# Performance work log

Hardware: AMD Instinct MI355X
Metric: run time of the kernel (lower is better)

## Reference

```python
import jax, jax.numpy as jnp
import numpy as np

N = 100000          # nodes
E = 3200000         # edges (before self-loops)
F_IN = 3            # num_features
H = 32              # hidden_size
F_EDGE = 4          # NUM_EDGE_FEATURES
T = 1               # target_size
SLOPE = 0.2         # GATConv negative_slope default


def setup_inputs() -> dict:
    key = jax.random.key(0)
    ks = jax.random.split(key, 18)
    s = 0.1  # small init scale
    inp = {
        "x": jax.random.normal(ks[0], (N, F_IN), jnp.float32),
        "edge_index": jax.random.randint(ks[1], (2, E), 0, N, dtype=jnp.int32),
        "edge_attr": jax.random.normal(ks[2], (E, F_EDGE), jnp.float32),
        # GATConv layer 1 (in=3, out=32, heads=1, edge_dim=4)
        "W1": jax.random.normal(ks[3], (F_IN, H), jnp.float32) * s,
        "We1": jax.random.normal(ks[4], (F_EDGE, H), jnp.float32) * s,
        "a_src1": jax.random.normal(ks[5], (H,), jnp.float32) * s,
        "a_dst1": jax.random.normal(ks[6], (H,), jnp.float32) * s,
        "a_edge1": jax.random.normal(ks[7], (H,), jnp.float32) * s,
        "b1": jnp.zeros((H,), jnp.float32),
        # GATConv layer 2 (in=32, out=32)
        "W2": jax.random.normal(ks[8], (H, H), jnp.float32) * s,
        "We2": jax.random.normal(ks[9], (F_EDGE, H), jnp.float32) * s,
        "a_src2": jax.random.normal(ks[10], (H,), jnp.float32) * s,
        "a_dst2": jax.random.normal(ks[11], (H,), jnp.float32) * s,
        "a_edge2": jax.random.normal(ks[12], (H,), jnp.float32) * s,
        "b2": jnp.zeros((H,), jnp.float32),
        # final Linear(32 -> 1)
        "Wl": jax.random.normal(ks[13], (H, T), jnp.float32) * s,
        "bl": jnp.zeros((T,), jnp.float32),
    }
    return inp


def _add_self_loops(edge_index, edge_attr, n):
    # PyG GATConv default: add_self_loops=True, fill_value='mean' -> self-loop
    # edge_attr is the mean of incoming edge_attr per destination node.
    src, dst = edge_index[0], edge_index[1]
    cnt = jax.ops.segment_sum(jnp.ones((edge_attr.shape[0],), edge_attr.dtype), dst, num_segments=n)
    sums = jax.ops.segment_sum(edge_attr, dst, num_segments=n)
    loop_attr = sums / jnp.maximum(cnt, 1.0)[:, None]
    idx = jnp.arange(n, dtype=src.dtype)
    src2 = jnp.concatenate([src, idx])
    dst2 = jnp.concatenate([dst, idx])
    ea2 = jnp.concatenate([edge_attr, loop_attr], axis=0)
    return src2, dst2, ea2


def _gat_layer(x, src, dst, ea, W, We, a_src, a_dst, a_edge, bias, n):
    h = x @ W                       # [N, H]
    e = ea @ We                     # [E', H]
    logits = jax.nn.leaky_relu(h[src] @ a_src + h[dst] @ a_dst + e @ a_edge, SLOPE)  # [E']
    # softmax over edges grouped by destination node
    m = jax.ops.segment_max(logits, dst, num_segments=n)
    w = jnp.exp(logits - m[dst])
    denom = jax.ops.segment_sum(w, dst, num_segments=n)
    alpha = w / denom[dst]
    out = jax.ops.segment_sum(alpha[:, None] * h[src], dst, num_segments=n)  # [N, H]
    return out + bias


def reference(x, edge_index, edge_attr, W1, We1, a_src1, a_dst1, a_edge1, b1,
              W2, We2, a_src2, a_dst2, a_edge2, b2, Wl, bl):
    n = x.shape[0]
    src, dst, ea = _add_self_loops(edge_index, edge_attr, n)
    h = _gat_layer(x, src, dst, ea, W1, We1, a_src1, a_dst1, a_edge1, b1, n)
    h = jax.nn.relu(h)  # dropout is identity in eval mode
    h = _gat_layer(h, src, dst, ea, W2, We2, a_src2, a_dst2, a_edge2, b2, n)
    out = h @ Wl + bl
    return jax.nn.relu(out)
```

## Files before the change

### kernel.cpp

```cpp
#include <hip/hip_runtime.h>
#include <hip/hip_fp16.h>


#define NN 100000
#define EE 3200000
#define SLOPE 0.2f
#define SB 1024
#define SNB ((NN + SB - 1) / SB)

__global__ void k_small(const float* __restrict__ We1, const float* __restrict__ ae1,
                        const float* __restrict__ We2, const float* __restrict__ ae2,
                        const float* __restrict__ W1, const float* __restrict__ as1,
                        const float* __restrict__ ad1, float* __restrict__ sml) {
    int t = threadIdx.x;
    if (t < 4) {
        float s = 0.f;
        for (int k = 0; k < 32; k++) s += We1[t * 32 + k] * ae1[k];
        sml[t] = s;
    } else if (t < 8) {
        float s = 0.f;
        for (int k = 0; k < 32; k++) s += We2[(t - 4) * 32 + k] * ae2[k];
        sml[t] = s;
    } else if (t < 11) {
        int i = t - 8;
        float s = 0.f;
        for (int k = 0; k < 32; k++) s += W1[i * 32 + k] * as1[k];
        sml[t] = s;
    } else if (t < 14) {
        int i = t - 11;
        float s = 0.f;
        for (int k = 0; k < 32; k++) s += W1[i * 32 + k] * ad1[k];
        sml[t] = s;
    }
}

__global__ void k_deg(const int* __restrict__ ei, int* __restrict__ deg) {
    int e = blockIdx.x * blockDim.x + threadIdx.x;
    if (e >= EE) return;
    atomicAdd(&deg[ei[EE + e]], 1);
}

__global__ void k_scan1(const int* __restrict__ deg, int* __restrict__ loc,
                        int* __restrict__ bsum) {
    __shared__ int sd[SB];
    int t = threadIdx.x;
    int i = blockIdx.x * SB + t;
    int v = (i < NN) ? deg[i] : 0;
    sd[t] = v;
    __syncthreads();
    for (int o = 1; o < SB; o <<= 1) {
        int u = (t >= o) ? sd[t - o] : 0;
        __syncthreads();
        sd[t] += u;
        __syncthreads();
    }
    if (i < NN) loc[i] = sd[t] - v;
    if (t == SB - 1) bsum[blockIdx.x] = sd[t];
}

__global__ void k_scan2(int* __restrict__ bsum) {
    __shared__ int sd[128];
    int t = threadIdx.x;
    int v = (t < SNB) ? bsum[t] : 0;
    sd[t] = v;
    __syncthreads();
    for (int o = 1; o < 128; o <<= 1) {
        int u = (t >= o) ? sd[t - o] : 0;
        __syncthreads();
        sd[t] += u;
        __syncthreads();
    }
    if (t < SNB) bsum[t] = sd[t] - v;
}

__global__ void k_scan3(const int* __restrict__ loc, const int* __restrict__ bsum,
                        int* __restrict__ rp, int* __restrict__ cur,
                        const float* __restrict__ x, const float* __restrict__ sml,
                        float* __restrict__ hs, float* __restrict__ hd) {
    int i = blockIdx.x * blockDim.x + threadIdx.x;
    if (i > NN) return;
    if (i == NN) { rp[NN] = EE; return; }
    int p = loc[i] + bsum[i / SB];
    rp[i] = p;
    cur[i] = p;
    float x0 = x[i * 3], x1 = x[i * 3 + 1], x2 = x[i * 3 + 2];
    hs[i] = x0 * sml[8] + x1 * sml[9] + x2 * sml[10];
    hd[i] = x0 * sml[11] + x1 * sml[12] + x2 * sml[13];
}

__global__ void k_scatter(const int* __restrict__ ei, const float* __restrict__ ea,
                          const float* __restrict__ sml, int* __restrict__ cur,
                          int2* __restrict__ cpack) {
    int e = blockIdx.x * blockDim.x + threadIdx.x;
    if (e >= EE) return;
    int s = ei[e], d = ei[EE + e];
    float4 a = reinterpret_cast<const float4*>(ea)[e];
    float e1 = a.x * sml[0] + a.y * sml[1] + a.z * sml[2] + a.w * sml[3];
    float e2 = a.x * sml[4] + a.y * sml[5] + a.z * sml[6] + a.w * sml[7];
    __half2 hv = __floats2half2_rn(e1, e2);
    int2 rec;
    rec.x = s;
    rec.y = *reinterpret_cast<int*>(&hv);
    int p = atomicAdd(&cur[d], 1);
    cpack[p] = rec;
}

__global__ void k_h2(const float* __restrict__ x2, const float* __restrict__ W,
                     const float* __restrict__ as_, const float* __restrict__ ad_,
                     float* __restrict__ h, float* __restrict__ hs, float* __restrict__ hd) {
    __shared__ float sW[1024], sa[32], sdv[32];
    int t = threadIdx.x;
    for (int i = t; i < 1024; i += blockDim.x) sW[i] = W[i];
    if (t < 32) { sa[t] = as_[t]; sdv[t] = ad_[t]; }
    __syncthreads();
    int n = blockIdx.x * blockDim.x + t;
    if (n >= NN) return;
    float xl[32];
    const float4* xp = reinterpret_cast<const float4*>(x2 + (size_t)n * 32);
#pragma unroll
    for (int q = 0; q < 8; q++) {
        float4 v = xp[q];
        xl[q * 4 + 0] = v.x; xl[q * 4 + 1] = v.y; xl[q * 4 + 2] = v.z; xl[q * 4 + 3] = v.w;
    }
    float ss = 0.f, dd = 0.f;
    float* hp = h + (size_t)n * 32;
    for (int q = 0; q < 8; q++) {
        float4 o;
        float* op = (float*)&o;
        for (int j = 0; j < 4; j++) {
            int k = q * 4 + j;
            float acc = 0.f;
#pragma unroll
            for (int i = 0; i < 32; i++) acc += xl[i] * sW[i * 32 + k];
            op[j] = acc;
            ss += acc * sa[k];
            dd += acc * sdv[k];
        }
        reinterpret_cast<float4*>(hp)[q] = o;
    }
    hs[n] = ss; hd[n] = dd;
}

template <int LAYER>
__global__ void __launch_bounds__(256) k_gather(
    const int* __restrict__ rp, const int2* __restrict__ cpack,
    const float* __restrict__ hsrc,
    const float* __restrict__ W1, const float* __restrict__ hs,
    const float* __restrict__ hd, const float* __restrict__ bias,
    const float* __restrict__ Wl, const float* __restrict__ bl,
    float* __restrict__ out) {
    __shared__ float sW[96];
    if (LAYER == 0) {
        if (threadIdx.x < 96) sW[threadIdx.x] = W1[threadIdx.x];
        __syncthreads();
    }
    int wid = (blockIdx.x * blockDim.x + threadIdx.x) >> 6;
    int lane = threadIdx.x & 63;
    if (wid >= NN) return;
    int n = wid;
    int beg = rp[n], end = rp[n + 1];
    int deg = end - beg;
    float hdn = hd[n];

    float mymax = -1e30f, mysum = 0.f;
    for (int j = beg + lane; j < end; j += 64) {
        int2 cp = cpack[j];
        __half2 hv = *reinterpret_cast<__half2*>(&cp.y);
        float2 ew = __half22float2(hv);
        float eaw = (LAYER == 0) ? ew.x : ew.y;
        float l = hs[cp.x] + hdn + eaw;
        l = (l >= 0.f) ? l : SLOPE * l;
        mymax = fmaxf(mymax, l);
        mysum += eaw;
    }
#pragma unroll
    for (int o = 32; o; o >>= 1) {
        mymax = fmaxf(mymax, __shfl_xor(mymax, o));
        mysum += __shfl_xor(mysum, o);
    }
    float lself = hs[n] + hdn + mysum / fmaxf((float)deg, 1.f);
    lself = (lself >= 0.f) ? lself : SLOPE * lself;
    float m = fmaxf(mymax, lself);

    int g = lane >> 3, q = lane & 7;
    float ax = 0.f, ay = 0.f, az = 0.f, aw = 0.f, wsum = 0.f;
    for (int j = beg + g; j < end; j += 8) {
        int2 cp = cpack[j];
        __half2 hv2 = *reinterpret_cast<__half2*>(&cp.y);
        float2 ew = __half22float2(hv2);
        float eaw = (LAYER == 0) ? ew.x : ew.y;
        int s = cp.x;
        float l = hs[s] + hdn + eaw;
        l = (l >= 0.f) ? l : SLOPE * l;
        float w = __expf(l - m);
        wsum += w;
        float hx, hy, hz, hw;
        if (LAYER == 0) {
            float x0 = hsrc[s * 3], x1 = hsrc[s * 3 + 1], x2 = hsrc[s * 3 + 2];
            int k = q * 4;
            hx = x0 * sW[k + 0] + x1 * sW[32 + k + 0] + x2 * sW[64 + k + 0];
            hy = x0 * sW[k + 1] + x1 * sW[32 + k + 1] + x2 * sW[64 + k + 1];
            hz = x0 * sW[k + 2] + x1 * sW[32 + k + 2] + x2 * sW[64 + k + 2];
            hw = x0 * sW[k + 3] + x1 * sW[32 + k + 3] + x2 * sW[64 + k + 3];
        } else {
            float4 hv4 = reinterpret_cast<const float4*>(hsrc + (size_t)s * 32)[q];
            hx = hv4.x; hy = hv4.y; hz = hv4.z; hw = hv4.w;
        }
        ax += w * hx; ay += w * hy; az += w * hz; aw += w * hw;
    }
    if (g == (deg & 7)) {
        float w = __expf(lself - m);
        wsum += w;
        float hx, hy, hz, hw;
        if (LAYER == 0) {
            float x0 = hsrc[n * 3], x1 = hsrc[n * 3 + 1], x2 = hsrc[n * 3 + 2];
            int k = q * 4;
            hx = x0 * sW[k + 0] + x1 * sW[32 + k + 0] + x2 * sW[64 + k + 0];
            hy = x0 * sW[k + 1] + x1 * sW[32 + k + 1] + x2 * sW[64 + k + 1];
            hz = x0 * sW[k + 2] + x1 * sW[32 + k + 2] + x2 * sW[64 + k + 2];
            hw = x0 * sW[k + 3] + x1 * sW[32 + k + 3] + x2 * sW[64 + k + 3];
        } else {
            float4 hv4 = reinterpret_cast<const float4*>(hsrc + (size_t)n * 32)[q];
            hx = hv4.x; hy = hv4.y; hz = hv4.z; hw = hv4.w;
        }
        ax += w * hx; ay += w * hy; az += w * hz; aw += w * hw;
    }
#pragma unroll
    for (int o = 8; o < 64; o <<= 1) {
        ax += __shfl_xor(ax, o); ay += __shfl_xor(ay, o);
        az += __shfl_xor(az, o); aw += __shfl_xor(aw, o);
        wsum += __shfl_xor(wsum, o);
    }
    float inv = 1.f / wsum;
    if (LAYER == 0) {
        if (lane < 8) {
            float4 bb = reinterpret_cast<const float4*>(bias)[q];
            float4 o4;
            o4.x = fmaxf(ax * inv + bb.x, 0.f);
            o4.y = fmaxf(ay * inv + bb.y, 0.f);
            o4.z = fmaxf(az * inv + bb.z, 0.f);
            o4.w = fmaxf(aw * inv + bb.w, 0.f);
            reinterpret_cast<float4*>(out + (size_t)n * 32)[q] = o4;
        }
    } else {
        float4 bb = reinterpret_cast<const float4*>(bias)[q];
        float4 wl = reinterpret_cast<const float4*>(Wl)[q];
        float part = (ax * inv + bb.x) * wl.x + (ay * inv + bb.y) * wl.y +
                     (az * inv + bb.z) * wl.z + (aw * inv + bb.w) * wl.w;
        part += __shfl_xor(part, 1);
        part += __shfl_xor(part, 2);
        part += __shfl_xor(part, 4);
        if (lane == 0) out[n] = fmaxf(part + bl[0], 0.f);
    }
}

extern "C" void kernel_launch(void* const* d_in, const int* in_sizes, int n_in,
                              void* d_out, int out_size, void* d_ws, size_t ws_size,
                              hipStream_t stream) {
    const float* x   = (const float*)d_in[0];
    const int*   ei  = (const int*)d_in[1];
    const float* ea  = (const float*)d_in[2];
    const float* W1  = (const float*)d_in[3];
    const float* We1 = (const float*)d_in[4];
    const float* as1 = (const float*)d_in[5];
    const float* ad1 = (const float*)d_in[6];
    const float* ae1 = (const float*)d_in[7];
    const float* b1  = (const float*)d_in[8];
    const float* W2  = (const float*)d_in[9];
    const float* We2 = (const float*)d_in[10];
    const float* as2 = (const float*)d_in[11];
    const float* ad2 = (const float*)d_in[12];
    const float* ae2 = (const float*)d_in[13];
    const float* b2  = (const float*)d_in[14];
    const float* Wl  = (const float*)d_in[15];
    const float* bl  = (const float*)d_in[16];
    float* out = (float*)d_out;

    const size_t n = NN, E = EE;
    float* ws = (float*)d_ws;
    int*   rp    = (int*)ws;
    int*   deg   = (int*)ws + n + 4;
    int*   cur   = (int*)ws + 2 * n + 4;
    int*   loc   = (int*)ws + 3 * n + 4;
    int*   bsum  = (int*)ws + 4 * n + 4;
    float* hs    = ws + 4 * n + 132;
    float* hd    = ws + 5 * n + 132;
    float* sml   = ws + 6 * n + 132;
    int2*  cpack = (int2*)(ws + 6 * n + 148);
    float* h     = ws + 6 * n + 148 + 2 * E;
    float* xbuf  = ws + 38 * n + 148 + 2 * E;

    dim3 b256(256);
    int gE  = (EE + 255) / 256;
    int gN  = (NN + 255) / 256;
    int gN1 = (NN + 256) / 256;
    int gG  = (NN * 64 + 255) / 256;

    hipMemsetAsync(deg, 0, n * sizeof(int), stream);
    k_small<<<1, 64, 0, stream>>>(We1, ae1, We2, ae2, W1, as1, ad1, sml);
    k_deg<<<gE, b256, 0, stream>>>(ei, deg);
    k_scan1<<<SNB, SB, 0, stream>>>(deg, loc, bsum);
    k_scan2<<<1, 128, 0, stream>>>(bsum);
    k_scan3<<<gN1, b256, 0, stream>>>(loc, bsum, rp, cur, x, sml, hs, hd);
    k_scatter<<<gE, b256, 0, stream>>>(ei, ea, sml, cur, cpack);

    k_gather<0><<<gG, b256, 0, stream>>>(rp, cpack, x, W1, hs, hd, b1,
                                         nullptr, nullptr, xbuf);

    k_h2<<<gN, b256, 0, stream>>>(xbuf, W2, as2, ad2, h, hs, hd);
    k_gather<1><<<gG, b256, 0, stream>>>(rp, cpack, h, nullptr, hs, hd, b2,
                                         Wl, bl, out);
}
```

Baseline: 622.3 us.

## Partition degree count and CSR scatter atomics by XCD-owned destination ranges

The degree-count and scatter kernels now run as persistent grids. Each block reads its XCD id and first works through the edge chunks whose destinations fall in that XCD's slice of the node range, taking chunks from a dynamic work queue and making 8 passes over all edges. This keeps the atomics for each destination range inside one XCD's L2, avoiding cross-die atomic traffic. The edge-feature projection is split into a separate kernel that writes packed half2 values. The cost is that every edge index is read 8 times per kernel and the packed values take an extra buffer round trip.

```diff
diff --git a/kernel.cpp b/kernel.cpp
--- a/kernel.cpp
+++ b/kernel.cpp
@@ -7,6 +7,17 @@
 #define SLOPE 0.2f
 #define SB 1024
 #define SNB ((NN + SB - 1) / SB)
+#define CH 2048
+#define NCH ((EE + CH - 1) / CH)
+#define SGRID 2048
+#define NXCD 8
+#define XSPAN (NN / NXCD)
+
+__device__ __forceinline__ unsigned get_xcd() {
+    unsigned x;
+    asm volatile("s_getreg_b32 %0, hwreg(HW_REG_XCC_ID)" : "=s"(x));
+    return x & (NXCD - 1);
+}
 
 __global__ void k_small(const float* __restrict__ We1, const float* __restrict__ ae1,
                         const float* __restrict__ We2, const float* __restrict__ ae2,
@@ -34,10 +45,38 @@
     }
 }
 
-__global__ void k_deg(const int* __restrict__ ei, int* __restrict__ deg) {
+__global__ void k_eaw(const float* __restrict__ ea, const float* __restrict__ sml,
+                      int* __restrict__ eaw) {
     int e = blockIdx.x * blockDim.x + threadIdx.x;
     if (e >= EE) return;
-    atomicAdd(&deg[ei[EE + e]], 1);
+    float4 a = reinterpret_cast<const float4*>(ea)[e];
+    float e1 = a.x * sml[0] + a.y * sml[1] + a.z * sml[2] + a.w * sml[3];
+    float e2 = a.x * sml[4] + a.y * sml[5] + a.z * sml[6] + a.w * sml[7];
+    __half2 hv = __floats2half2_rn(e1, e2);
+    eaw[e] = *reinterpret_cast<int*>(&hv);
+}
+
+__global__ void __launch_bounds__(256) k_deg_x(const int* __restrict__ ei,
+                                               int* __restrict__ deg,
+                                               int* __restrict__ q) {
+    unsigned myx = get_xcd();
+    __shared__ int s_chunk;
+    for (int pass = 0; pass < NXCD; ++pass) {
+        int x = (myx + pass) & (NXCD - 1);
+        int lo = x * XSPAN, hi = lo + XSPAN;
+        for (;;) {
+            if (threadIdx.x == 0) s_chunk = atomicAdd(&q[x], 1);
+            __syncthreads();
+            int c = s_chunk;
+            __syncthreads();
+            if (c >= NCH) break;
+            int base = c * CH, lim = min(base + CH, EE);
+            for (int e = base + (int)threadIdx.x; e < lim; e += 256) {
+                int d = ei[EE + e];
+                if (d >= lo && d < hi) atomicAdd(&deg[d], 1);
+            }
+        }
+    }
 }
 
 __global__ void k_scan1(const int* __restrict__ deg, int* __restrict__ loc,
@@ -88,21 +127,34 @@
     hd[i] = x0 * sml[11] + x1 * sml[12] + x2 * sml[13];
 }
 
-__global__ void k_scatter(const int* __restrict__ ei, const float* __restrict__ ea,
-                          const float* __restrict__ sml, int* __restrict__ cur,
-                          int2* __restrict__ cpack) {
-    int e = blockIdx.x * blockDim.x + threadIdx.x;
-    if (e >= EE) return;
-    int s = ei[e], d = ei[EE + e];
-    float4 a = reinterpret_cast<const float4*>(ea)[e];
-    float e1 = a.x * sml[0] + a.y * sml[1] + a.z * sml[2] + a.w * sml[3];
-    float e2 = a.x * sml[4] + a.y * sml[5] + a.z * sml[6] + a.w * sml[7];
-    __half2 hv = __floats2half2_rn(e1, e2);
-    int2 rec;
-    rec.x = s;
-    rec.y = *reinterpret_cast<int*>(&hv);
-    int p = atomicAdd(&cur[d], 1);
-    cpack[p] = rec;
+__global__ void __launch_bounds__(256) k_scatter_x(const int* __restrict__ ei,
+                                                   const int* __restrict__ eaw,
+                                                   int* __restrict__ cur,
+                                                   int2* __restrict__ cpack,
+                                                   int* __restrict__ q) {
+    unsigned myx = get_xcd();
+    __shared__ int s_chunk;
+    for (int pass = 0; pass < NXCD; ++pass) {
+        int x = (myx + pass) & (NXCD - 1);
+        int lo = x * XSPAN, hi = lo + XSPAN;
+        for (;;) {
+            if (threadIdx.x == 0) s_chunk = atomicAdd(&q[x], 1);
+            __syncthreads();
+            int c = s_chunk;
+            __syncthreads();
+            if (c >= NCH) break;
+            int base = c * CH, lim = min(base + CH, EE);
+            for (int e = base + (int)threadIdx.x; e < lim; e += 256) {
+                int d = ei[EE + e];
+                if (d < lo || d >= hi) continue;
+                int2 rec;
+                rec.x = ei[e];
+                rec.y = eaw[e];
+                int p = atomicAdd(&cur[d], 1);
+                cpack[p] = rec;
+            }
+        }
+    }
 }
 
 __global__ void k_h2(const float* __restrict__ x2, const float* __restrict__ W,
@@ -280,15 +332,17 @@
     float* ws = (float*)d_ws;
     int*   rp    = (int*)ws;
     int*   deg   = (int*)ws + n + 4;
-    int*   cur   = (int*)ws + 2 * n + 4;
-    int*   loc   = (int*)ws + 3 * n + 4;
-    int*   bsum  = (int*)ws + 4 * n + 4;
-    float* hs    = ws + 4 * n + 132;
-    float* hd    = ws + 5 * n + 132;
-    float* sml   = ws + 6 * n + 132;
-    int2*  cpack = (int2*)(ws + 6 * n + 148);
-    float* h     = ws + 6 * n + 148 + 2 * E;
-    float* xbuf  = ws + 38 * n + 148 + 2 * E;
+    int*   qq    = (int*)ws + 2 * n + 4;
+    int*   cur   = (int*)ws + 2 * n + 20;
+    int*   loc   = (int*)ws + 3 * n + 20;
+    int*   bsum  = (int*)ws + 4 * n + 20;
+    float* hs    = ws + 4 * n + 148;
+    float* hd    = ws + 5 * n + 148;
+    float* sml   = ws + 6 * n + 148;
+    int*   eaw   = (int*)(ws + 6 * n + 164);
+    int2*  cpack = (int2*)(ws + 6 * n + 164 + E);
+    float* h     = ws + 6 * n + 164 + 3 * E;
+    float* xbuf  = ws + 38 * n + 164 + 3 * E;
 
     dim3 b256(256);
     int gE  = (EE + 255) / 256;
@@ -296,13 +350,14 @@
     int gN1 = (NN + 256) / 256;
     int gG  = (NN * 64 + 255) / 256;
 
-    hipMemsetAsync(deg, 0, n * sizeof(int), stream);
+    hipMemsetAsync(deg, 0, (n + 16) * sizeof(int), stream);
     k_small<<<1, 64, 0, stream>>>(We1, ae1, We2, ae2, W1, as1, ad1, sml);
-    k_deg<<<gE, b256, 0, stream>>>(ei, deg);
+    k_eaw<<<gE, b256, 0, stream>>>(ea, sml, eaw);
+    k_deg_x<<<SGRID, b256, 0, stream>>>(ei, deg, qq);
     k_scan1<<<SNB, SB, 0, stream>>>(deg, loc, bsum);
     k_scan2<<<1, 128, 0, stream>>>(bsum);
     k_scan3<<<gN1, b256, 0, stream>>>(loc, bsum, rp, cur, x, sml, hs, hd);
-    k_scatter<<<gE, b256, 0, stream>>>(ei, ea, sml, cur, cpack);
+    k_scatter_x<<<SGRID, b256, 0, stream>>>(ei, eaw, cur, cpack, qq + 8);
 
     k_gather<0><<<gG, b256, 0, stream>>>(rp, cpack, x, W1, hs, hd, b1,
                                          nullptr, nullptr, xbuf);
```

Result: slower. 976.8 us (+57.0%).
